# Kernel tuning notes

Measured on AMD Instinct MI355X. Metric: run time of the kernel, lower is better.

Reference implementation:

```python
import jax, jax.numpy as jnp
import numpy as np

N = 100000   # nodes
E = 1600000  # edges
R = 500      # relation types
D = 128      # in_ent_feats == out_ent_feats
H = 8        # heads
Dh = 16      # head dim
DFF = 4 * D  # feed-forward hidden
HOPS = 5
ALPHA = 0.15
SLOPE = 0.2
EPS = 1e-5


def setup_inputs() -> dict:
    key = jax.random.key(0)
    ks = jax.random.split(key, 12)
    s = 0.05  # small-init scale
    return {
        "ent_feat": jax.random.normal(ks[0], (N, D), jnp.float32),
        "rel_feat": jax.random.normal(ks[1], (R, D), jnp.float32),
        "src": jax.random.randint(ks[2], (E,), 0, N),
        "dst": jax.random.randint(ks[3], (E,), 0, N),
        "e_type": jax.random.randint(ks[4], (E,), 0, R),
        "ln1_g": jnp.ones((D,), jnp.float32),
        "ln1_b": jnp.zeros((D,), jnp.float32),
        "W_ent": jax.random.normal(ks[5], (D, H * Dh), jnp.float32) * s,
        "W_rel": jax.random.normal(ks[6], (D, H * Dh), jnp.float32) * s,
        "attn_h": jax.random.normal(ks[7], (1, H, Dh), jnp.float32) * s,
        "attn_t": jax.random.normal(ks[8], (1, H, Dh), jnp.float32) * s,
        "attn_r": jax.random.normal(ks[9], (1, H, Dh), jnp.float32) * s,
        "ln2_g": jnp.ones((H * Dh,), jnp.float32),
        "ln2_b": jnp.zeros((H * Dh,), jnp.float32),
        "W1": jax.random.normal(ks[10], (H * Dh, DFF), jnp.float32) * s,
        "b1": jnp.zeros((DFF,), jnp.float32),
        "W2": jax.random.normal(ks[11], (DFF, H * Dh), jnp.float32) * s,
        "b2": jnp.zeros((H * Dh,), jnp.float32),
    }


def _ln(x, g, b):
    mu = x.mean(-1, keepdims=True)
    var = x.var(-1, keepdims=True)
    return (x - mu) * jax.lax.rsqrt(var + EPS) * g + b


def reference(ent_feat, rel_feat, src, dst, e_type,
              ln1_g, ln1_b, W_ent, W_rel, attn_h, attn_t, attn_r,
              ln2_g, ln2_b, W1, b1, W2, b2):
    # graph layer norm (dropout is identity at eval)
    h = _ln(ent_feat, ln1_g, ln1_b)                       # [N, D]
    feat = (h @ W_ent).reshape(N, H, Dh)                  # [N, H, Dh]
    frel = (rel_feat @ W_rel).reshape(R, H, Dh)           # [R, H, Dh]
    eh = (feat * attn_h).sum(-1)                          # [N, H]
    et = (feat * attn_t).sum(-1)                          # [N, H]
    er = (frel * attn_r).sum(-1)[e_type]                  # [E, H]
    # edge scores: u_add_v + relation term, leaky relu
    e = eh[src] + et[dst] + er                            # [E, H]
    e = jnp.where(e > 0, e, SLOPE * e)
    # edge softmax over incoming edges of each dst node
    m = jax.ops.segment_max(e, dst, num_segments=N)       # [N, H]
    ex = jnp.exp(e - m[dst])
    ssum = jax.ops.segment_sum(ex, dst, num_segments=N)
    a = ex / ssum[dst]                                    # [E, H]
    # PPR diffusion
    feat0 = feat
    f = feat0
    for _ in range(HOPS):
        msg = f[src] * a[:, :, None]                      # [E, H, Dh]
        agg = jax.ops.segment_sum(msg, dst, num_segments=N)
        f = (1.0 - ALPHA) * agg + ALPHA * feat0
    # residual (Identity since in == out)
    rst = f + h.reshape(N, H, Dh)
    rst = rst.reshape(N, H * Dh)
    # feed-forward sublayer with residual
    y = _ln(rst, ln2_g, ln2_b)
    ff = jax.nn.relu(y @ W1 + b1) @ W2 + b2
    return ff + rst
```

## Files before the change

### kernel.cpp

```cpp
#include <hip/hip_runtime.h>
#include <hip/hip_bf16.h>
#include <math.h>

#define N_NODES 100000
#define N_EDGES 1600000
#define N_REL   500
#define DIM     128
#define NHEAD   8
#define DFF     512
#define ALPHA   0.15f
#define SLOPE   0.2f
#define LN_EPS  1e-5f

#define SCHUNK   1024
#define NSCANBLK ((N_NODES + SCHUNK - 1) / SCHUNK)

typedef unsigned short u16;
typedef unsigned int   u32;

typedef __attribute__((ext_vector_type(8))) short  bf16x8;
typedef __attribute__((ext_vector_type(4))) float  f32x4;

__device__ __forceinline__ float bf2f(u16 u) {
    return __uint_as_float(((u32)u) << 16);
}
__device__ __forceinline__ u16 f2bf(float f) {
    __hip_bfloat16 b = __float2bfloat16(f);
    return *reinterpret_cast<u16*>(&b);
}
__device__ __forceinline__ u32 pack2(float a, float b) {
    return (u32)f2bf(a) | ((u32)f2bf(b) << 16);
}

__global__ void zero_k(int* __restrict__ p, int n) {
    int i = blockIdx.x * blockDim.x + threadIdx.x;
    if (i < n) p[i] = 0;
}

__global__ void swz1_k(const float* __restrict__ W1, u16* __restrict__ W1s) {
    const int i = blockIdx.x * 256 + threadIdx.x;
    const int k = i >> 9, n = i & 511;
    W1s[n * DIM + k] = f2bf(W1[i]);
}
__global__ void swz2_k(const float* __restrict__ W2, u16* __restrict__ W2s) {
    const int i = blockIdx.x * 256 + threadIdx.x;
    const int k = i >> 7, n = i & 127;
    W2s[n * DFF + k] = f2bf(W2[i]);
}
__global__ void swze_k(const float* __restrict__ W, u16* __restrict__ Ws) {
    const int i = blockIdx.x * 256 + threadIdx.x;
    const int k = i >> 7, n = i & 127;
    Ws[n * DIM + k] = f2bf(W[i]);
}

__global__ __launch_bounds__(128) void ln1_k(const float* __restrict__ x,
        const float* __restrict__ g, const float* __restrict__ b,
        float* __restrict__ h) {
    const int n = blockIdx.x, t = threadIdx.x;
    const float v = x[n * DIM + t];
    float s = v, q = v * v;
#pragma unroll
    for (int off = 32; off > 0; off >>= 1) {
        s += __shfl_xor(s, off, 64);
        q += __shfl_xor(q, off, 64);
    }
    __shared__ float ss[2], qq[2];
    if ((t & 63) == 0) { ss[t >> 6] = s; qq[t >> 6] = q; }
    __syncthreads();
    s = ss[0] + ss[1]; q = qq[0] + qq[1];
    const float mu  = s * (1.0f / 128.0f);
    const float var = q * (1.0f / 128.0f) - mu * mu;
    const float rs  = rsqrtf(fmaxf(var, 0.f) + LN_EPS);
    h[n * DIM + t] = (v - mu) * rs * g[t] + b[t];
}

#define HP 136
__global__ __launch_bounds__(256) void proj_k(const float* __restrict__ h,
        const u16* __restrict__ Wes,
        u16* __restrict__ feat0) {
    __shared__ u16 hsb[32 * HP];
    const int t   = threadIdx.x;
    const int n0b = blockIdx.x * 32;

    {
        const int sr = t >> 3;
        const int sc = (t & 7) * 16;
        const float* hrow = &h[(size_t)(n0b + sr) * DIM + sc];
        u16* drow = &hsb[sr * HP + sc];
#pragma unroll
        for (int i = 0; i < 4; ++i) {
            const float4 hv = ((const float4*)hrow)[i];
            ushort4 o;
            o.x = f2bf(hv.x); o.y = f2bf(hv.y); o.z = f2bf(hv.z); o.w = f2bf(hv.w);
            ((ushort4*)drow)[i] = o;
        }
    }
    __syncthreads();

    const int wv   = t >> 6;
    const int lane = t & 63;
    const int lm   = lane & 15;
    const int q4   = lane >> 4;
    const int mrow = (wv & 1) * 16;
    const int chalf = (wv >> 1) * 64;

    bf16x8 afr[4];
#pragma unroll
    for (int kt = 0; kt < 4; ++kt)
        afr[kt] = *(const bf16x8*)&hsb[(mrow + lm) * HP + kt * 32 + q4 * 8];

#pragma unroll
    for (int nt = 0; nt < 4; ++nt) {
        const int c0 = chalf + nt * 16;
        f32x4 acc = {0.f, 0.f, 0.f, 0.f};
#pragma unroll
        for (int kt = 0; kt < 4; ++kt) {
            const bf16x8 bfr = *(const bf16x8*)&Wes[(c0 + lm) * DIM + kt * 32 + q4 * 8];
            acc = __builtin_amdgcn_mfma_f32_16x16x32_bf16(afr[kt], bfr, acc, 0, 0, 0);
        }
#pragma unroll
        for (int r = 0; r < 4; ++r)
            feat0[(size_t)(n0b + mrow + q4 * 4 + r) * DIM + c0 + lm] = f2bf(acc[r]);
    }
}

__global__ __launch_bounds__(256) void eh_k(const u16* __restrict__ feat0,
        const float* __restrict__ attn_h, const float* __restrict__ attn_t,
        float* __restrict__ eh, float* __restrict__ et) {
    __shared__ float ahs[DIM], ats[DIM];
    const int t = threadIdx.x;
    if (t < DIM) { ahs[t] = attn_h[t]; ats[t] = attn_t[t]; }
    __syncthreads();
    const int idx  = blockIdx.x * 256 + t;
    const int n    = idx >> 3;
    const int head = idx & 7;
    const u16* fp = &feat0[(size_t)n * DIM + head * 16];
    float sh = 0.f, st = 0.f;
#pragma unroll
    for (int i = 0; i < 4; ++i) {
        const ushort4 f4 = ((const ushort4*)fp)[i];
        const int c = head * 16 + i * 4;
        sh += bf2f(f4.x) * ahs[c+0] + bf2f(f4.y) * ahs[c+1]
            + bf2f(f4.z) * ahs[c+2] + bf2f(f4.w) * ahs[c+3];
        st += bf2f(f4.x) * ats[c+0] + bf2f(f4.y) * ats[c+1]
            + bf2f(f4.z) * ats[c+2] + bf2f(f4.w) * ats[c+3];
    }
    eh[idx] = sh;
    et[idx] = st;
}

__global__ __launch_bounds__(128) void rel_k(const float* __restrict__ rel_feat,
        const float* __restrict__ W,
        const float* __restrict__ attn_r, float* __restrict__ er) {
    __shared__ float rf[DIM];
    __shared__ float pr[DIM];
    const int r = blockIdx.x, t = threadIdx.x;
    rf[t] = rel_feat[r * DIM + t];
    __syncthreads();
    float acc = 0.f;
    for (int d = 0; d < DIM; ++d) acc += rf[d] * W[d * DIM + t];
    pr[t] = acc * attn_r[t];
    __syncthreads();
    if (t < NHEAD) {
        float s = 0.f;
        for (int i = 0; i < 16; ++i) s += pr[t * 16 + i];
        er[r * NHEAD + t] = s;
    }
}

__global__ void count_k(const int* __restrict__ dst, int* __restrict__ counts) {
    int e = blockIdx.x * blockDim.x + threadIdx.x;
    if (e < N_EDGES) atomicAdd(&counts[dst[e]], 1);
}

__global__ __launch_bounds__(256) void scan1_k(const int* __restrict__ counts,
        int* __restrict__ offsets, int* __restrict__ blk_sums, int n) {
    __shared__ int wsum[4];
    const int t = threadIdx.x, lane = t & 63, wid = t >> 6;
    const int base = blockIdx.x * SCHUNK + t * 4;
    int v0 = 0, v1 = 0, v2 = 0, v3 = 0;
    if (base + 3 < n) {
        const int4 c4 = *(const int4*)&counts[base];
        v0 = c4.x; v1 = c4.y; v2 = c4.z; v3 = c4.w;
    } else {
        if (base + 0 < n) v0 = counts[base + 0];
        if (base + 1 < n) v1 = counts[base + 1];
        if (base + 2 < n) v2 = counts[base + 2];
        if (base + 3 < n) v3 = counts[base + 3];
    }
    const int s4 = v0 + v1 + v2 + v3;
    int incl = s4;
#pragma unroll
    for (int off = 1; off < 64; off <<= 1) {
        const int tt = __shfl_up(incl, off, 64);
        if (lane >= off) incl += tt;
    }
    if (lane == 63) wsum[wid] = incl;
    __syncthreads();
    int wbase = 0;
#pragma unroll
    for (int w = 0; w < 4; ++w) if (w < wid) wbase += wsum[w];
    const int excl = wbase + incl - s4;
    if (base + 0 < n) offsets[base + 0] = excl;
    if (base + 1 < n) offsets[base + 1] = excl + v0;
    if (base + 2 < n) offsets[base + 2] = excl + v0 + v1;
    if (base + 3 < n) offsets[base + 3] = excl + v0 + v1 + v2;
    if (t == 255) blk_sums[blockIdx.x] = wbase + incl;
}

__global__ __launch_bounds__(128) void scan2_k(const int* __restrict__ blk_sums,
        int* __restrict__ blk_off, int* __restrict__ offsets, int nblk, int n) {
    const int t = threadIdx.x;
    const int v = (t < nblk) ? blk_sums[t] : 0;
    int incl = v;
#pragma unroll
    for (int off = 1; off < 64; off <<= 1) {
        const int tt = __shfl_up(incl, off, 64);
        if ((t & 63) >= off) incl += tt;
    }
    __shared__ int w0sum;
    if (t == 63) w0sum = incl;
    __syncthreads();
    int x = incl - v;
    if (t >= 64) x += w0sum;
    if (t < nblk) blk_off[t] = x;
    if (t == nblk - 1) offsets[n] = x + v;
}

__global__ __launch_bounds__(256) void scan3_k(int* __restrict__ offsets,
        int* __restrict__ cursor, const int* __restrict__ blk_off, int n) {
    const int add  = blk_off[blockIdx.x];
    const int base = blockIdx.x * SCHUNK + threadIdx.x * 4;
#pragma unroll
    for (int j = 0; j < 4; ++j) {
        const int i = base + j;
        if (i < n) {
            const int o = offsets[i] + add;
            offsets[i] = o;
            cursor[i]  = o;
        }
    }
}

__global__ void scatter_k(const int* __restrict__ src, const int* __restrict__ dst,
        const int* __restrict__ etype,
        const float* __restrict__ eh, const float* __restrict__ et,
        const float* __restrict__ er,
        int* __restrict__ cursor, int* __restrict__ csr_src,
        u16* __restrict__ csr_ab) {
    const int e = blockIdx.x * blockDim.x + threadIdx.x;
    if (e >= N_EDGES) return;
    const int s = src[e], d = dst[e], r = etype[e];
    const float4 h0 = *(const float4*)&eh[s * NHEAD];
    const float4 h1 = *(const float4*)&eh[s * NHEAD + 4];
    const float4 t0 = *(const float4*)&et[d * NHEAD];
    const float4 t1 = *(const float4*)&et[d * NHEAD + 4];
    const float4 r0 = *(const float4*)&er[r * NHEAD];
    const float4 r1 = *(const float4*)&er[r * NHEAD + 4];
    float4 a0, a1;
    a0.x = h0.x + t0.x + r0.x; a0.y = h0.y + t0.y + r0.y;
    a0.z = h0.z + t0.z + r0.z; a0.w = h0.w + t0.w + r0.w;
    a1.x = h1.x + t1.x + r1.x; a1.y = h1.y + t1.y + r1.y;
    a1.z = h1.z + t1.z + r1.z; a1.w = h1.w + t1.w + r1.w;
    a0.x = a0.x > 0.f ? a0.x : SLOPE * a0.x;
    a0.y = a0.y > 0.f ? a0.y : SLOPE * a0.y;
    a0.z = a0.z > 0.f ? a0.z : SLOPE * a0.z;
    a0.w = a0.w > 0.f ? a0.w : SLOPE * a0.w;
    a1.x = a1.x > 0.f ? a1.x : SLOPE * a1.x;
    a1.y = a1.y > 0.f ? a1.y : SLOPE * a1.y;
    a1.z = a1.z > 0.f ? a1.z : SLOPE * a1.z;
    a1.w = a1.w > 0.f ? a1.w : SLOPE * a1.w;
    const int pos = atomicAdd(&cursor[d], 1);
    if (pos < 0 || pos >= N_EDGES) return;
    csr_src[pos] = s;
    uint4 packed;
    packed.x = pack2(a0.x, a0.y);
    packed.y = pack2(a0.z, a0.w);
    packed.z = pack2(a1.x, a1.y);
    packed.w = pack2(a1.z, a1.w);
    *(uint4*)&csr_ab[(size_t)pos * NHEAD] = packed;
}

__global__ __launch_bounds__(256) void softmax_k(const int* __restrict__ offsets,
        u16* __restrict__ csr_ab, float* __restrict__ inv_buf) {
    const int n = blockIdx.x * 4 + (threadIdx.x >> 6);
    const int beg = offsets[n], end = offsets[n + 1];
    const int lane = threadIdx.x & 63;
    const int k  = lane & 7;
    const int eo = lane >> 3;
    float m = -1e30f;
    for (int e = beg + eo; e < end; e += 8)
        m = fmaxf(m, bf2f(csr_ab[(size_t)e * NHEAD + k]));
    m = fmaxf(m, __shfl_xor(m, 8, 64));
    m = fmaxf(m, __shfl_xor(m, 16, 64));
    m = fmaxf(m, __shfl_xor(m, 32, 64));
    float ssum = 0.f;
    for (int e = beg + eo; e < end; e += 8) {
        const float ex = expf(bf2f(csr_ab[(size_t)e * NHEAD + k]) - m);
        csr_ab[(size_t)e * NHEAD + k] = f2bf(ex);
        ssum += ex;
    }
    ssum += __shfl_xor(ssum, 8, 64);
    ssum += __shfl_xor(ssum, 16, 64);
    ssum += __shfl_xor(ssum, 32, 64);
    const float inv = 1.f / fmaxf(ssum, 1e-20f);
    if (lane < 8) inv_buf[n * NHEAD + lane] = inv;
}

__global__ __launch_bounds__(256) void hop_k(const u16* f_in,
        u16* __restrict__ f_out, const u16* feat0,
        const int* __restrict__ offsets, const int* __restrict__ csr_src,
        const u16* __restrict__ csr_ab, const float* __restrict__ inv_buf) {
    const int n    = blockIdx.x * 4 + (threadIdx.x >> 6);
    const int lane = threadIdx.x & 63;
    const int beg = offsets[n], end = offsets[n + 1];
    const int hsel = lane >> 3;
    const int d2   = lane << 1;
    float2 acc = {0.f, 0.f};
    int e = beg;
    for (; e + 4 <= end; e += 4) {
        const int s0 = csr_src[e + 0];
        const int s1 = csr_src[e + 1];
        const int s2 = csr_src[e + 2];
        const int s3 = csr_src[e + 3];
        const float a0 = bf2f(csr_ab[(size_t)(e + 0) * NHEAD + hsel]);
        const float a1 = bf2f(csr_ab[(size_t)(e + 1) * NHEAD + hsel]);
        const float a2 = bf2f(csr_ab[(size_t)(e + 2) * NHEAD + hsel]);
        const float a3 = bf2f(csr_ab[(size_t)(e + 3) * NHEAD + hsel]);
        const ushort2 w0 = *(const ushort2*)&f_in[s0 * DIM + d2];
        const ushort2 w1 = *(const ushort2*)&f_in[s1 * DIM + d2];
        const ushort2 w2 = *(const ushort2*)&f_in[s2 * DIM + d2];
        const ushort2 w3 = *(const ushort2*)&f_in[s3 * DIM + d2];
        acc.x += a0 * bf2f(w0.x) + a1 * bf2f(w1.x) + a2 * bf2f(w2.x) + a3 * bf2f(w3.x);
        acc.y += a0 * bf2f(w0.y) + a1 * bf2f(w1.y) + a2 * bf2f(w2.y) + a3 * bf2f(w3.y);
    }
    for (; e < end; ++e) {
        const int s0 = csr_src[e];
        const float a0 = bf2f(csr_ab[(size_t)e * NHEAD + hsel]);
        const ushort2 w0 = *(const ushort2*)&f_in[s0 * DIM + d2];
        acc.x += a0 * bf2f(w0.x);
        acc.y += a0 * bf2f(w0.y);
    }
    const float iv = inv_buf[n * NHEAD + hsel];
    const ushort2 p = *(const ushort2*)&feat0[n * DIM + d2];
    const float ox = (1.f - ALPHA) * acc.x * iv + ALPHA * bf2f(p.x);
    const float oy = (1.f - ALPHA) * acc.y * iv + ALPHA * bf2f(p.y);
    ushort2 o; o.x = f2bf(ox); o.y = f2bf(oy);
    *(ushort2*)&f_out[n * DIM + d2] = o;
}

#define YP 136
#define ZP 520
__global__ __launch_bounds__(256) void ffn_k(const u16* __restrict__ f,
        const float* __restrict__ h,
        const float* __restrict__ g2, const float* __restrict__ b2ln,
        const u16* __restrict__ W1s,
        const float* __restrict__ b1,
        const u16* __restrict__ W2s,
        const float* __restrict__ b2,
        float* __restrict__ out) {
    __shared__ u16 ysb[32 * YP];
    __shared__ u16 zsb[32 * ZP];
    __shared__ float red[32][8];
    __shared__ float red2[32][8];
    __shared__ float mu_s[32], rs_s[32];

    const int t   = threadIdx.x;
    const int n0b = blockIdx.x * 32;

    const int an = t >> 3;
    const int ap = t & 7;
    float rv[16];
    {
        const int gbase = (n0b + an) * DIM + ap * 16;
#pragma unroll
        for (int i = 0; i < 4; ++i) {
            const ushort4 fu = *(const ushort4*)&f[gbase + i * 4];
            const float4  hv = *(const float4*)&h[gbase + i * 4];
            rv[i * 4 + 0] = bf2f(fu.x) + hv.x;
            rv[i * 4 + 1] = bf2f(fu.y) + hv.y;
            rv[i * 4 + 2] = bf2f(fu.z) + hv.z;
            rv[i * 4 + 3] = bf2f(fu.w) + hv.w;
        }
        float s = 0.f, q = 0.f;
#pragma unroll
        for (int i = 0; i < 16; ++i) { s += rv[i]; q += rv[i] * rv[i]; }
        red[an][ap] = s; red2[an][ap] = q;
    }
    __syncthreads();
    if (t < 32) {
        float s = 0.f, q = 0.f;
#pragma unroll
        for (int i = 0; i < 8; ++i) { s += red[t][i]; q += red2[t][i]; }
        const float mu  = s * (1.0f / 128.0f);
        const float var = q * (1.0f / 128.0f) - mu * mu;
        mu_s[t] = mu;
        rs_s[t] = rsqrtf(fmaxf(var, 0.f) + LN_EPS);
    }
    __syncthreads();
    {
        const float mu = mu_s[an], rs = rs_s[an];
#pragma unroll
        for (int i = 0; i < 4; ++i) {
            ushort4 yo;
            const int c = ap * 16 + i * 4;
            yo.x = f2bf((rv[i*4+0] - mu) * rs * g2[c+0] + b2ln[c+0]);
            yo.y = f2bf((rv[i*4+1] - mu) * rs * g2[c+1] + b2ln[c+1]);
            yo.z = f2bf((rv[i*4+2] - mu) * rs * g2[c+2] + b2ln[c+2]);
            yo.w = f2bf((rv[i*4+3] - mu) * rs * g2[c+3] + b2ln[c+3]);
            *(ushort4*)&ysb[an * YP + c] = yo;
        }
    }
    __syncthreads();

    const int wv   = t >> 6;
    const int lane = t & 63;
    const int lm   = lane & 15;
    const int q4   = lane >> 4;

    bf16x8 afr[2][4];
#pragma unroll
    for (int mt = 0; mt < 2; ++mt)
#pragma unroll
        for (int kt = 0; kt < 4; ++kt)
            afr[mt][kt] = *(const bf16x8*)&ysb[(mt * 16 + lm) * YP + kt * 32 + q4 * 8];

    for (int nt = 0; nt < 8; ++nt) {
        const int n0 = wv * 128 + nt * 16;
        f32x4 acc0 = {0.f, 0.f, 0.f, 0.f};
        f32x4 acc1 = {0.f, 0.f, 0.f, 0.f};
#pragma unroll
        for (int kt = 0; kt < 4; ++kt) {
            const bf16x8 bfr = *(const bf16x8*)&W1s[(n0 + lm) * DIM + kt * 32 + q4 * 8];
            acc0 = __builtin_amdgcn_mfma_f32_16x16x32_bf16(afr[0][kt], bfr, acc0, 0, 0, 0);
            acc1 = __builtin_amdgcn_mfma_f32_16x16x32_bf16(afr[1][kt], bfr, acc1, 0, 0, 0);
        }
        const float bias = b1[n0 + lm];
#pragma unroll
        for (int r = 0; r < 4; ++r) {
            zsb[(q4 * 4 + r) * ZP + n0 + lm]        = f2bf(fmaxf(acc0[r] + bias, 0.f));
            zsb[(16 + q4 * 4 + r) * ZP + n0 + lm]   = f2bf(fmaxf(acc1[r] + bias, 0.f));
        }
    }
    __syncthreads();

    f32x4 acc[2][2];
#pragma unroll
    for (int i = 0; i < 2; ++i)
#pragma unroll
        for (int j = 0; j < 2; ++j)
            acc[i][j] = (f32x4){0.f, 0.f, 0.f, 0.f};
    const int c0 = wv * 32;
    for (int kt = 0; kt < 16; ++kt) {
        const bf16x8 a0 = *(const bf16x8*)&zsb[(lm) * ZP + kt * 32 + q4 * 8];
        const bf16x8 a1 = *(const bf16x8*)&zsb[(16 + lm) * ZP + kt * 32 + q4 * 8];
        const bf16x8 b0 = *(const bf16x8*)&W2s[(c0 + lm) * DFF + kt * 32 + q4 * 8];
        const bf16x8 b1f = *(const bf16x8*)&W2s[(c0 + 16 + lm) * DFF + kt * 32 + q4 * 8];
        acc[0][0] = __builtin_amdgcn_mfma_f32_16x16x32_bf16(a0, b0, acc[0][0], 0, 0, 0);
        acc[0][1] = __builtin_amdgcn_mfma_f32_16x16x32_bf16(a0, b1f, acc[0][1], 0, 0, 0);
        acc[1][0] = __builtin_amdgcn_mfma_f32_16x16x32_bf16(a1, b0, acc[1][0], 0, 0, 0);
        acc[1][1] = __builtin_amdgcn_mfma_f32_16x16x32_bf16(a1, b1f, acc[1][1], 0, 0, 0);
    }

#pragma unroll
    for (int ntile = 0; ntile < 2; ++ntile) {
        const int col = c0 + ntile * 16 + lm;
        const float bias = b2[col];
#pragma unroll
        for (int mt = 0; mt < 2; ++mt) {
#pragma unroll
            for (int r = 0; r < 4; ++r) {
                const int row  = mt * 16 + q4 * 4 + r;
                const int gidx = (n0b + row) * DIM + col;
                out[gidx] = acc[mt][ntile][r] + bias + bf2f(f[gidx]) + h[gidx];
            }
        }
    }
}

extern "C" void kernel_launch(void* const* d_in, const int* in_sizes, int n_in,
                              void* d_out, int out_size, void* d_ws, size_t ws_size,
                              hipStream_t stream) {
    const float* ent_feat = (const float*)d_in[0];
    const float* rel_feat = (const float*)d_in[1];
    const int*   src      = (const int*)d_in[2];
    const int*   dst      = (const int*)d_in[3];
    const int*   e_type   = (const int*)d_in[4];
    const float* ln1_g    = (const float*)d_in[5];
    const float* ln1_b    = (const float*)d_in[6];
    const float* W_ent    = (const float*)d_in[7];
    const float* W_rel    = (const float*)d_in[8];
    const float* attn_h   = (const float*)d_in[9];
    const float* attn_t   = (const float*)d_in[10];
    const float* attn_r   = (const float*)d_in[11];
    const float* ln2_g    = (const float*)d_in[12];
    const float* ln2_b    = (const float*)d_in[13];
    const float* W1       = (const float*)d_in[14];
    const float* b1       = (const float*)d_in[15];
    const float* W2       = (const float*)d_in[16];
    const float* b2       = (const float*)d_in[17];
    float* out = (float*)d_out;

    char* ws = (char*)d_ws;
    size_t used = 0;
    auto alloc = [&](size_t bytes) -> char* {
        char* p = ws + used;
        used += (bytes + 255) & ~(size_t)255;
        return p;
    };
    float* h       = (float*)alloc((size_t)N_NODES * DIM * 4);
    u16*   feat0   = (u16*)  alloc((size_t)N_NODES * DIM * 2);
    u16*   fA      = (u16*)  alloc((size_t)N_NODES * DIM * 2);
    u16*   fB      = (u16*)  alloc((size_t)N_NODES * DIM * 2);
    u16*   csr_ab  = (u16*)  alloc((size_t)N_EDGES * NHEAD * 2);
    float* eh      = (float*)alloc((size_t)N_NODES * NHEAD * 4);
    float* et      = (float*)alloc((size_t)N_NODES * NHEAD * 4);
    float* inv_buf = (float*)alloc((size_t)N_NODES * NHEAD * 4);
    int*   csr_src = (int*)  alloc((size_t)N_EDGES * 4);
    int*   counts  = (int*)  alloc((size_t)N_NODES * 4);
    int*   offsets = (int*)  alloc((size_t)(N_NODES + 1) * 4);
    int*   cursor  = (int*)  alloc((size_t)N_NODES * 4);
    float* er      = (float*)alloc((size_t)N_REL * NHEAD * 4);
    u16*   W1s     = (u16*)  alloc((size_t)DIM * DFF * 2);
    u16*   W2s     = (u16*)  alloc((size_t)DFF * DIM * 2);
    u16*   Wes     = (u16*)  alloc((size_t)DIM * DIM * 2);
    int*   blk_sums= (int*)  alloc((size_t)NSCANBLK * 4);
    int*   blk_off = (int*)  alloc((size_t)NSCANBLK * 4);

    if (used > ws_size) return;

    swz1_k<<<DIM * DFF / 256, 256, 0, stream>>>(W1, W1s);
    swz2_k<<<DFF * DIM / 256, 256, 0, stream>>>(W2, W2s);
    swze_k<<<DIM * DIM / 256, 256, 0, stream>>>(W_ent, Wes);

    ln1_k<<<N_NODES, 128, 0, stream>>>(ent_feat, ln1_g, ln1_b, h);
    proj_k<<<N_NODES / 32, 256, 0, stream>>>(h, Wes, feat0);
    eh_k<<<N_NODES * NHEAD / 256, 256, 0, stream>>>(feat0, attn_h, attn_t, eh, et);
    rel_k<<<N_REL, 128, 0, stream>>>(rel_feat, W_rel, attn_r, er);

    zero_k<<<(N_NODES + 255) / 256, 256, 0, stream>>>(counts, N_NODES);
    count_k<<<(N_EDGES + 255) / 256, 256, 0, stream>>>(dst, counts);
    scan1_k<<<NSCANBLK, 256, 0, stream>>>(counts, offsets, blk_sums, N_NODES);
    scan2_k<<<1, 128, 0, stream>>>(blk_sums, blk_off, offsets, NSCANBLK, N_NODES);
    scan3_k<<<NSCANBLK, 256, 0, stream>>>(offsets, cursor, blk_off, N_NODES);
    scatter_k<<<(N_EDGES + 255) / 256, 256, 0, stream>>>(src, dst, e_type, eh, et, er,
                                                         cursor, csr_src, csr_ab);
    softmax_k<<<N_NODES / 4, 256, 0, stream>>>(offsets, csr_ab, inv_buf);

    hop_k<<<N_NODES / 4, 256, 0, stream>>>(feat0, fA, feat0, offsets, csr_src, csr_ab, inv_buf);
    hop_k<<<N_NODES / 4, 256, 0, stream>>>(fA, fB, feat0, offsets, csr_src, csr_ab, inv_buf);
    hop_k<<<N_NODES / 4, 256, 0, stream>>>(fB, fA, feat0, offsets, csr_src, csr_ab, inv_buf);
    hop_k<<<N_NODES / 4, 256, 0, stream>>>(fA, fB, feat0, offsets, csr_src, csr_ab, inv_buf);
    hop_k<<<N_NODES / 4, 256, 0, stream>>>(fB, fA, feat0, offsets, csr_src, csr_ab, inv_buf);

    ffn_k<<<N_NODES / 32, 256, 0, stream>>>(fA, h, ln2_g, ln2_b, W1s, b1, W2s, b2,
                                            out);
}
```

Baseline: 954.3 us.

## Pack src and edge type into CSR, compute scores in softmax, widen hop gathers

The scatter kernel now writes only a packed (src, relation) word per edge. Edge scores are computed inside the softmax kernel from eh/et/er, which removes the bf16 score write in scatter and its reread. The hop kernel is restructured so 16 lanes each load a 16-byte bf16x8 slice of a source row while 4 lane groups handle different edges, followed by a cross-group shuffle reduction. This replaces narrow 4-byte gathers with wider ones, at the cost of recomputing scores twice in softmax, more registers, and only 16 lanes active in the epilogue.

```diff
diff --git a/kernel.cpp b/kernel.cpp
--- a/kernel.cpp
+++ b/kernel.cpp
@@ -244,59 +244,46 @@
 
 __global__ void scatter_k(const int* __restrict__ src, const int* __restrict__ dst,
         const int* __restrict__ etype,
-        const float* __restrict__ eh, const float* __restrict__ et,
-        const float* __restrict__ er,
-        int* __restrict__ cursor, int* __restrict__ csr_src,
-        u16* __restrict__ csr_ab) {
+        int* __restrict__ cursor, u32* __restrict__ csr_se) {
     const int e = blockIdx.x * blockDim.x + threadIdx.x;
     if (e >= N_EDGES) return;
     const int s = src[e], d = dst[e], r = etype[e];
-    const float4 h0 = *(const float4*)&eh[s * NHEAD];
-    const float4 h1 = *(const float4*)&eh[s * NHEAD + 4];
-    const float4 t0 = *(const float4*)&et[d * NHEAD];
-    const float4 t1 = *(const float4*)&et[d * NHEAD + 4];
-    const float4 r0 = *(const float4*)&er[r * NHEAD];
-    const float4 r1 = *(const float4*)&er[r * NHEAD + 4];
-    float4 a0, a1;
-    a0.x = h0.x + t0.x + r0.x; a0.y = h0.y + t0.y + r0.y;
-    a0.z = h0.z + t0.z + r0.z; a0.w = h0.w + t0.w + r0.w;
-    a1.x = h1.x + t1.x + r1.x; a1.y = h1.y + t1.y + r1.y;
-    a1.z = h1.z + t1.z + r1.z; a1.w = h1.w + t1.w + r1.w;
-    a0.x = a0.x > 0.f ? a0.x : SLOPE * a0.x;
-    a0.y = a0.y > 0.f ? a0.y : SLOPE * a0.y;
-    a0.z = a0.z > 0.f ? a0.z : SLOPE * a0.z;
-    a0.w = a0.w > 0.f ? a0.w : SLOPE * a0.w;
-    a1.x = a1.x > 0.f ? a1.x : SLOPE * a1.x;
-    a1.y = a1.y > 0.f ? a1.y : SLOPE * a1.y;
-    a1.z = a1.z > 0.f ? a1.z : SLOPE * a1.z;
-    a1.w = a1.w > 0.f ? a1.w : SLOPE * a1.w;
     const int pos = atomicAdd(&cursor[d], 1);
     if (pos < 0 || pos >= N_EDGES) return;
-    csr_src[pos] = s;
-    uint4 packed;
-    packed.x = pack2(a0.x, a0.y);
-    packed.y = pack2(a0.z, a0.w);
-    packed.z = pack2(a1.x, a1.y);
-    packed.w = pack2(a1.z, a1.w);
-    *(uint4*)&csr_ab[(size_t)pos * NHEAD] = packed;
+    csr_se[pos] = (u32)s | ((u32)r << 17);
 }
 
 __global__ __launch_bounds__(256) void softmax_k(const int* __restrict__ offsets,
+        const u32* __restrict__ csr_se,
+        const float* __restrict__ eh, const float* __restrict__ et,
+        const float* __restrict__ er,
         u16* __restrict__ csr_ab, float* __restrict__ inv_buf) {
     const int n = blockIdx.x * 4 + (threadIdx.x >> 6);
     const int beg = offsets[n], end = offsets[n + 1];
     const int lane = threadIdx.x & 63;
     const int k  = lane & 7;
     const int eo = lane >> 3;
+    const float etk = et[n * NHEAD + k];
     float m = -1e30f;
-    for (int e = beg + eo; e < end; e += 8)
-        m = fmaxf(m, bf2f(csr_ab[(size_t)e * NHEAD + k]));
+    for (int e = beg + eo; e < end; e += 8) {
+        const u32 se = csr_se[e];
+        const int s = se & 0x1FFFF;
+        const int r = se >> 17;
+        float sc = eh[s * NHEAD + k] + etk + er[r * NHEAD + k];
+        sc = sc > 0.f ? sc : SLOPE * sc;
+        m = fmaxf(m, sc);
+    }
     m = fmaxf(m, __shfl_xor(m, 8, 64));
     m = fmaxf(m, __shfl_xor(m, 16, 64));
     m = fmaxf(m, __shfl_xor(m, 32, 64));
     float ssum = 0.f;
     for (int e = beg + eo; e < end; e += 8) {
-        const float ex = expf(bf2f(csr_ab[(size_t)e * NHEAD + k]) - m);
+        const u32 se = csr_se[e];
+        const int s = se & 0x1FFFF;
+        const int r = se >> 17;
+        float sc = eh[s * NHEAD + k] + etk + er[r * NHEAD + k];
+        sc = sc > 0.f ? sc : SLOPE * sc;
+        const float ex = expf(sc - m);
         csr_ab[(size_t)e * NHEAD + k] = f2bf(ex);
         ssum += ex;
     }
@@ -307,46 +294,61 @@
     if (lane < 8) inv_buf[n * NHEAD + lane] = inv;
 }
 
-__global__ __launch_bounds__(256) void hop_k(const u16* f_in,
-        u16* __restrict__ f_out, const u16* feat0,
-        const int* __restrict__ offsets, const int* __restrict__ csr_src,
+__global__ __launch_bounds__(256) void hop_k(const u16* __restrict__ f_in,
+        u16* __restrict__ f_out, const u16* __restrict__ feat0,
+        const int* __restrict__ offsets, const u32* __restrict__ csr_se,
         const u16* __restrict__ csr_ab, const float* __restrict__ inv_buf) {
     const int n    = blockIdx.x * 4 + (threadIdx.x >> 6);
     const int lane = threadIdx.x & 63;
+    const int li   = lane & 15;
+    const int grp  = lane >> 4;
+    const int hsel = li >> 1;
     const int beg = offsets[n], end = offsets[n + 1];
-    const int hsel = lane >> 3;
-    const int d2   = lane << 1;
-    float2 acc = {0.f, 0.f};
-    int e = beg;
-    for (; e + 4 <= end; e += 4) {
-        const int s0 = csr_src[e + 0];
-        const int s1 = csr_src[e + 1];
-        const int s2 = csr_src[e + 2];
-        const int s3 = csr_src[e + 3];
-        const float a0 = bf2f(csr_ab[(size_t)(e + 0) * NHEAD + hsel]);
-        const float a1 = bf2f(csr_ab[(size_t)(e + 1) * NHEAD + hsel]);
-        const float a2 = bf2f(csr_ab[(size_t)(e + 2) * NHEAD + hsel]);
-        const float a3 = bf2f(csr_ab[(size_t)(e + 3) * NHEAD + hsel]);
-        const ushort2 w0 = *(const ushort2*)&f_in[s0 * DIM + d2];
-        const ushort2 w1 = *(const ushort2*)&f_in[s1 * DIM + d2];
-        const ushort2 w2 = *(const ushort2*)&f_in[s2 * DIM + d2];
-        const ushort2 w3 = *(const ushort2*)&f_in[s3 * DIM + d2];
-        acc.x += a0 * bf2f(w0.x) + a1 * bf2f(w1.x) + a2 * bf2f(w2.x) + a3 * bf2f(w3.x);
-        acc.y += a0 * bf2f(w0.y) + a1 * bf2f(w1.y) + a2 * bf2f(w2.y) + a3 * bf2f(w3.y);
-    }
-    for (; e < end; ++e) {
-        const int s0 = csr_src[e];
-        const float a0 = bf2f(csr_ab[(size_t)e * NHEAD + hsel]);
-        const ushort2 w0 = *(const ushort2*)&f_in[s0 * DIM + d2];
-        acc.x += a0 * bf2f(w0.x);
-        acc.y += a0 * bf2f(w0.y);
-    }
-    const float iv = inv_buf[n * NHEAD + hsel];
-    const ushort2 p = *(const ushort2*)&feat0[n * DIM + d2];
-    const float ox = (1.f - ALPHA) * acc.x * iv + ALPHA * bf2f(p.x);
-    const float oy = (1.f - ALPHA) * acc.y * iv + ALPHA * bf2f(p.y);
-    ushort2 o; o.x = f2bf(ox); o.y = f2bf(oy);
-    *(ushort2*)&f_out[n * DIM + d2] = o;
+    const int deg = end - beg;
+
+    float acc[8];
+#pragma unroll
+    for (int j = 0; j < 8; ++j) acc[j] = 0.f;
+
+    const int nfull = deg >> 4;
+    int e0 = beg;
+    for (int i = 0; i < nfull; ++i, e0 += 16) {
+        const u32 se16 = csr_se[e0 + li];
+#pragma unroll
+        for (int u = 0; u < 4; ++u) {
+            const int eu = e0 + u * 4 + grp;
+            const u32 se = __shfl(se16, u * 4 + grp, 16);
+            const int s  = (int)(se & 0x1FFFF);
+            const float a = bf2f(csr_ab[(size_t)eu * NHEAD + hsel]);
+            const bf16x8 row = *(const bf16x8*)&f_in[(size_t)s * DIM + li * 8];
+#pragma unroll
+            for (int j = 0; j < 8; ++j)
+                acc[j] += a * bf2f((u16)row[j]);
+        }
+    }
+    for (int e = e0 + grp; e < end; e += 4) {
+        const u32 se = csr_se[e];
+        const int s  = (int)(se & 0x1FFFF);
+        const float a = bf2f(csr_ab[(size_t)e * NHEAD + hsel]);
+        const bf16x8 row = *(const bf16x8*)&f_in[(size_t)s * DIM + li * 8];
+#pragma unroll
+        for (int j = 0; j < 8; ++j)
+            acc[j] += a * bf2f((u16)row[j]);
+    }
+#pragma unroll
+    for (int j = 0; j < 8; ++j) {
+        acc[j] += __shfl_xor(acc[j], 16, 64);
+        acc[j] += __shfl_xor(acc[j], 32, 64);
+    }
+    if (lane < 16) {
+        const float iv = inv_buf[n * NHEAD + hsel];
+        const bf16x8 p = *(const bf16x8*)&feat0[(size_t)n * DIM + li * 8];
+        bf16x8 o;
+#pragma unroll
+        for (int j = 0; j < 8; ++j)
+            o[j] = (short)f2bf((1.f - ALPHA) * acc[j] * iv + ALPHA * bf2f((u16)p[j]));
+        *(bf16x8*)&f_out[(size_t)n * DIM + li * 8] = o;
+    }
 }
 
 #define YP 136
@@ -516,7 +518,7 @@
     float* eh      = (float*)alloc((size_t)N_NODES * NHEAD * 4);
     float* et      = (float*)alloc((size_t)N_NODES * NHEAD * 4);
     float* inv_buf = (float*)alloc((size_t)N_NODES * NHEAD * 4);
-    int*   csr_src = (int*)  alloc((size_t)N_EDGES * 4);
+    u32*   csr_se  = (u32*)  alloc((size_t)N_EDGES * 4);
     int*   counts  = (int*)  alloc((size_t)N_NODES * 4);
     int*   offsets = (int*)  alloc((size_t)(N_NODES + 1) * 4);
     int*   cursor  = (int*)  alloc((size_t)N_NODES * 4);
@@ -543,15 +545,16 @@
     scan1_k<<<NSCANBLK, 256, 0, stream>>>(counts, offsets, blk_sums, N_NODES);
     scan2_k<<<1, 128, 0, stream>>>(blk_sums, blk_off, offsets, NSCANBLK, N_NODES);
     scan3_k<<<NSCANBLK, 256, 0, stream>>>(offsets, cursor, blk_off, N_NODES);
-    scatter_k<<<(N_EDGES + 255) / 256, 256, 0, stream>>>(src, dst, e_type, eh, et, er,
-                                                         cursor, csr_src, csr_ab);
-    softmax_k<<<N_NODES / 4, 256, 0, stream>>>(offsets, csr_ab, inv_buf);
-
-    hop_k<<<N_NODES / 4, 256, 0, stream>>>(feat0, fA, feat0, offsets, csr_src, csr_ab, inv_buf);
-    hop_k<<<N_NODES / 4, 256, 0, stream>>>(fA, fB, feat0, offsets, csr_src, csr_ab, inv_buf);
-    hop_k<<<N_NODES / 4, 256, 0, stream>>>(fB, fA, feat0, offsets, csr_src, csr_ab, inv_buf);
-    hop_k<<<N_NODES / 4, 256, 0, stream>>>(fA, fB, feat0, offsets, csr_src, csr_ab, inv_buf);
-    hop_k<<<N_NODES / 4, 256, 0, stream>>>(fB, fA, feat0, offsets, csr_src, csr_ab, inv_buf);
+    scatter_k<<<(N_EDGES + 255) / 256, 256, 0, stream>>>(src, dst, e_type,
+                                                         cursor, csr_se);
+    softmax_k<<<N_NODES / 4, 256, 0, stream>>>(offsets, csr_se, eh, et, er,
+                                               csr_ab, inv_buf);
+
+    hop_k<<<N_NODES / 4, 256, 0, stream>>>(feat0, fA, feat0, offsets, csr_se, csr_ab, inv_buf);
+    hop_k<<<N_NODES / 4, 256, 0, stream>>>(fA, fB, feat0, offsets, csr_se, csr_ab, inv_buf);
+    hop_k<<<N_NODES / 4, 256, 0, stream>>>(fB, fA, feat0, offsets, csr_se, csr_ab, inv_buf);
+    hop_k<<<N_NODES / 4, 256, 0, stream>>>(fA, fB, feat0, offsets, csr_se, csr_ab, inv_buf);
+    hop_k<<<N_NODES / 4, 256, 0, stream>>>(fB, fA, feat0, offsets, csr_se, csr_ab, inv_buf);
 
     ffn_k<<<N_NODES / 32, 256, 0, stream>>>(fA, h, ln2_g, ln2_b, W1s, b1, W2s, b2,
                                             out);
```

New measurement: 932.6 us. 2.3% less time.
